# Performance work log

Measured on AMD Instinct MI355X. Metric: run time of the kernel, lower is better.

The kernel has to match this reference:

```python
import jax, jax.numpy as jnp
import numpy as np

B, S, HID, NH, HD, RD, RATIO = 2, 4096, 2048, 16, 128, 64, 4
THETA = 10000.0


def _rope_tables(positions, rd, theta):
    # Unique per-pair frequencies: first half of the Llama cat([freqs, freqs], -1).
    half = rd // 2
    inv_freq = 1.0 / (theta ** (jnp.arange(half, dtype=jnp.float32) / half))
    ang = positions.astype(jnp.float32)[:, None] * inv_freq[None, :]  # [L, half]
    return jnp.cos(ang), jnp.sin(ang)


def _apply_partial_rope_interleaved(x, cos, sin, rd):
    # x: [B, H, L, D]; rotate last rd dims, pairs (2k, 2k+1). cos/sin: [L, rd//2]
    nope, rope = x[..., :-rd], x[..., -rd:]
    pr = rope.reshape(rope.shape[:-1] + (rd // 2, 2))
    a, b = pr[..., 0], pr[..., 1]
    c = cos[None, None]  # [1,1,L,half]
    s = sin[None, None]
    new = jnp.stack([a * c - b * s, a * s + b * c], axis=-1).reshape(rope.shape)
    return jnp.concatenate([nope, new], axis=-1)


def _pool_overlap(kv, gate, ape, ratio, hd):
    # kv/gate: [B, L, 2*hd]; ape: [ratio, 2*hd]. Softmax-gated sum-pool with
    # cross-window overlap: each window pools 2*ratio raw slots (prev window's
    # first-half features + current window's second-half features).
    b, length, feat = kv.shape
    n_w = length // ratio
    kv_w = kv.reshape(b, n_w, ratio, feat)
    gate_w = gate.reshape(b, n_w, ratio, feat) + ape

    def remap(t, fill):
        cur = t[..., hd:]                          # [b, n_w, ratio, hd]
        prev = t[:, :-1, :, :hd]                   # window N-1 first half
        pad = jnp.full((b, 1, ratio, hd), fill, t.dtype)
        prev = jnp.concatenate([pad, prev], axis=1)
        return jnp.concatenate([prev, cur], axis=2)  # [b, n_w, 2*ratio, hd]

    kv_o = remap(kv_w, 0.0)
    gate_o = remap(gate_w, -jnp.inf)
    w = jax.nn.softmax(gate_o, axis=2)
    return (kv_o * w).sum(axis=2)  # [b, n_w, hd]


def setup_inputs() -> dict:
    key = jax.random.key(0)
    ks = jax.random.split(key, 7)
    sc = lambda d: 1.0 / np.sqrt(d)
    return {
        "hidden": jax.random.normal(ks[0], (B, S, HID), jnp.float32),
        "wq": jax.random.normal(ks[1], (HID, NH * HD), jnp.float32) * sc(HID),
        "wkv": jax.random.normal(ks[2], (HID, 2 * HD), jnp.float32) * sc(HID),
        "wgate": jax.random.normal(ks[3], (HID, 2 * HD), jnp.float32) * sc(HID),
        "ape": jax.random.normal(ks[4], (RATIO, 2 * HD), jnp.float32) * 0.02,
        "sinks": jax.random.normal(ks[5], (NH,), jnp.float32) * 0.02,
        "wo": jax.random.normal(ks[6], (NH * HD, HID), jnp.float32) * sc(NH * HD),
        "ratio": RATIO,
        "head_dim": HD,
        "rope_head_dim": RD,
        "num_heads": NH,
    }


def reference(hidden, wq, wkv, wgate, ape, sinks, wo, ratio, head_dim, rope_head_dim, num_heads):
    b, s, _ = hidden.shape
    scale = head_dim ** -0.5

    # Projections
    q = (hidden @ wq).reshape(b, s, num_heads, head_dim).transpose(0, 2, 1, 3)  # [b,h,s,d]
    kv = hidden @ wkv      # [b, s, 2*d]
    gate = hidden @ wgate  # [b, s, 2*d]

    # Overlap gated pooling -> compressed shared KV  [b, n_w, d]
    pooled = _pool_overlap(kv, gate, ape, ratio, head_dim)
    n_w = pooled.shape[1]

    # Partial interleaved RoPE; pooled positions = w * ratio (pool_base = 0)
    q_pos = jnp.arange(s)
    k_pos = jnp.arange(n_w) * ratio
    cq, sq = _rope_tables(q_pos, rope_head_dim, THETA)
    ck, sk = _rope_tables(k_pos, rope_head_dim, THETA)
    q_rot = _apply_partial_rope_interleaved(q, cq, sq, rope_head_dim)
    k_rot = _apply_partial_rope_interleaved(pooled[:, None], ck, sk, rope_head_dim)[:, 0]  # [b,n_w,d]
    v = pooled  # [b, n_w, d]

    # Causal mask over compressed windows: query t sees window w iff its last
    # raw token (w+1)*ratio - 1 <= t.
    mask = jnp.where(q_pos[:, None] >= k_pos[None, :] + ratio - 1, 0.0, -jnp.inf)  # [s, n_w]

    scores = jnp.einsum("bhqd,bkd->bhqk", q_rot, k_rot) * scale + mask[None, None]
    sink_col = jnp.broadcast_to(sinks.reshape(1, num_heads, 1, 1), (b, num_heads, s, 1))
    combined = jnp.concatenate([scores, sink_col], axis=-1)
    probs = jax.nn.softmax(combined - jax.lax.stop_gradient(combined.max(axis=-1, keepdims=True)), axis=-1)[..., :-1]

    attn = jnp.einsum("bhqk,bkd->bhqd", probs, v)               # [b,h,s,d]
    out = attn.transpose(0, 2, 1, 3).reshape(b, s, num_heads * head_dim) @ wo
    return out
```

## Files before the change

### kernel.cpp

```cpp
#include <hip/hip_runtime.h>
#include <math.h>

typedef unsigned short u16;
typedef unsigned int   u32;
typedef __bf16 bf16x8 __attribute__((ext_vector_type(8)));
typedef float  f32x4  __attribute__((ext_vector_type(4)));

#define S_LEN 4096
#define HID   2048
#define NHEAD 16
#define HD    128
#define NW    1024
#define TOK   8192
#define LN10000 9.2103403719761836f
#define NEG_BIG (-1e30f)

__device__ __forceinline__ float b2f(u16 u){
  union { u32 i; float f; } v; v.i = ((u32)u) << 16; return v.f;
}
__device__ __forceinline__ u16 f2b(float f){
  union { float f; u32 i; } v; v.f = f;
  return (u16)((v.i + 0x7FFFu + ((v.i >> 16) & 1u)) >> 16);
}

__global__ __launch_bounds__(256) void cvt_bf16(const float* __restrict__ in,
                                                u16* __restrict__ out){
  size_t i = (size_t)blockIdx.x*256 + threadIdx.x;
  float4 a = ((const float4*)in)[2*i];
  float4 b = ((const float4*)in)[2*i+1];
  u16 t[8];
  t[0]=f2b(a.x); t[1]=f2b(a.y); t[2]=f2b(a.z); t[3]=f2b(a.w);
  t[4]=f2b(b.x); t[5]=f2b(b.y); t[6]=f2b(b.z); t[7]=f2b(b.w);
  *(uint4*)&out[i*8] = *(uint4*)t;
}

__global__ __launch_bounds__(256) void transpose_w(const float* __restrict__ in,
    u16* __restrict__ out, int K, int N){
  __shared__ float t[32][33];
  const int n0 = blockIdx.x*32, k0 = blockIdx.y*32;
  const int c = threadIdx.x & 31, r8 = threadIdx.x >> 5;
  #pragma unroll
  for (int i = 0; i < 4; i++)
    t[r8 + i*8][c] = in[(size_t)(k0 + r8 + i*8)*N + n0 + c];
  __syncthreads();
  #pragma unroll
  for (int i = 0; i < 4; i++)
    out[(size_t)(n0 + r8 + i*8)*K + k0 + c] = f2b(t[c][r8 + i*8]);
}

typedef __attribute__((address_space(3))) u16 as3_u16;
typedef __attribute__((address_space(1))) const u16 as1_u16;
__device__ __forceinline__ void gload16(const u16* g, u16* l){
  __builtin_amdgcn_global_load_lds((as1_u16*)g, (as3_u16*)l, 16, 0, 0);
}

template<typename TC>
__global__ __launch_bounds__(512, 1) void gemm256(const u16* __restrict__ A,
    const u16* __restrict__ Bt, TC* __restrict__ C, int M, int N, int K)
{
  __shared__ __align__(16) u16 LA[2][256*64];
  __shared__ __align__(16) u16 LB[2][256*64];
  const int tid  = threadIdx.x;
  const int lane = tid & 63;
  const int w    = tid >> 6;
  const int wm   = w & 1;
  const int wn   = w >> 1;
  const int lrw  = lane & 15;
  const int quad = lane >> 4;
  const int NB   = N >> 8;
  const int nwg  = gridDim.x;
  const int bid  = blockIdx.x;
  const int swz  = (bid & 7) * (nwg >> 3) + (bid >> 3);
  const int bN   = (swz % NB) << 8;
  const int bM   = (swz / NB) << 8;

  const int rlo = lane >> 3;
  const int csw = ((lane & 7) ^ rlo) << 3;
  const int sr0 = w * 16;
  const int swr = (lrw & 7) << 3;
  const u16* Ag = A  + (size_t)bM * K + (size_t)rlo * K + csw;
  const u16* Bg = Bt + (size_t)bN * K + (size_t)rlo * K + csw;
  const size_t rK = (size_t)K;

  f32x4 acc[8][4];
  #pragma unroll
  for (int i = 0; i < 8; i++)
    #pragma unroll
    for (int j = 0; j < 4; j++)
      #pragma unroll
      for (int r = 0; r < 4; r++) acc[i][j][r] = 0.f;

  const int NT = K >> 6;

  gload16(Ag + (size_t)(  0 + sr0    )*rK, &LA[0][(  0 + sr0    )*64]);
  gload16(Ag + (size_t)(  0 + sr0 + 8)*rK, &LA[0][(  0 + sr0 + 8)*64]);
  gload16(Bg + (size_t)(  0 + sr0    )*rK, &LB[0][(  0 + sr0    )*64]);
  gload16(Bg + (size_t)(  0 + sr0 + 8)*rK, &LB[0][(  0 + sr0 + 8)*64]);
  gload16(Bg + (size_t)(128 + sr0    )*rK, &LB[0][(128 + sr0    )*64]);
  gload16(Bg + (size_t)(128 + sr0 + 8)*rK, &LB[0][(128 + sr0 + 8)*64]);
  gload16(Ag + (size_t)(128 + sr0    )*rK, &LA[0][(128 + sr0    )*64]);
  gload16(Ag + (size_t)(128 + sr0 + 8)*rK, &LA[0][(128 + sr0 + 8)*64]);
  asm volatile("s_waitcnt vmcnt(2)" ::: "memory");
  __builtin_amdgcn_s_barrier();
  __builtin_amdgcn_sched_barrier(0);

  for (int t = 0; t < NT; ++t){
    const int cur = t & 1, nxt = cur ^ 1;
    const int kn  = ((t + 1) & (NT - 1)) << 6;
    const u16* la = &LA[cur][0];
    const u16* lb = &LB[cur][0];
    u16* sa = &LA[nxt][0];
    u16* sb = &LB[nxt][0];

    bf16x8 bfr[4][2], afr[2][2];

    gload16(Ag + (size_t)(  0 + sr0    )*rK + kn, &sa[(  0 + sr0    )*64]);
    gload16(Ag + (size_t)(  0 + sr0 + 8)*rK + kn, &sa[(  0 + sr0 + 8)*64]);
    gload16(Bg + (size_t)(  0 + sr0    )*rK + kn, &sb[(  0 + sr0    )*64]);
    gload16(Bg + (size_t)(  0 + sr0 + 8)*rK + kn, &sb[(  0 + sr0 + 8)*64]);
    #pragma unroll
    for (int nf = 0; nf < 4; nf++)
      #pragma unroll
      for (int kh = 0; kh < 2; kh++)
        bfr[nf][kh] = *(const bf16x8*)&lb[(wn*16 + nf*64 + lrw)*64 + ((kh*32 + quad*8) ^ swr)];
    #pragma unroll
    for (int i = 0; i < 2; i++)
      #pragma unroll
      for (int kh = 0; kh < 2; kh++)
        afr[i][kh] = *(const bf16x8*)&la[(wm*16 + (0+i)*32 + lrw)*64 + ((kh*32 + quad*8) ^ swr)];
    __builtin_amdgcn_s_barrier();
    __builtin_amdgcn_sched_barrier(0);
    __builtin_amdgcn_s_setprio(1);
    #pragma unroll
    for (int i = 0; i < 2; i++)
      #pragma unroll
      for (int nf = 0; nf < 4; nf++)
        #pragma unroll
        for (int kh = 0; kh < 2; kh++)
          acc[0+i][nf] = __builtin_amdgcn_mfma_f32_16x16x32_bf16(afr[i][kh], bfr[nf][kh], acc[0+i][nf], 0, 0, 0);
    __builtin_amdgcn_s_setprio(0);
    __builtin_amdgcn_s_barrier();
    __builtin_amdgcn_sched_barrier(0);

    gload16(Bg + (size_t)(128 + sr0    )*rK + kn, &sb[(128 + sr0    )*64]);
    gload16(Bg + (size_t)(128 + sr0 + 8)*rK + kn, &sb[(128 + sr0 + 8)*64]);
    #pragma unroll
    for (int i = 0; i < 2; i++)
      #pragma unroll
      for (int kh = 0; kh < 2; kh++)
        afr[i][kh] = *(const bf16x8*)&la[(wm*16 + (2+i)*32 + lrw)*64 + ((kh*32 + quad*8) ^ swr)];
    asm volatile("s_waitcnt vmcnt(6)" ::: "memory");
    __builtin_amdgcn_s_barrier();
    __builtin_amdgcn_sched_barrier(0);
    __builtin_amdgcn_s_setprio(1);
    #pragma unroll
    for (int i = 0; i < 2; i++)
      #pragma unroll
      for (int nf = 0; nf < 4; nf++)
        #pragma unroll
        for (int kh = 0; kh < 2; kh++)
          acc[2+i][nf] = __builtin_amdgcn_mfma_f32_16x16x32_bf16(afr[i][kh], bfr[nf][kh], acc[2+i][nf], 0, 0, 0);
    __builtin_amdgcn_s_setprio(0);
    __builtin_amdgcn_s_barrier();
    __builtin_amdgcn_sched_barrier(0);

    gload16(Ag + (size_t)(128 + sr0    )*rK + kn, &sa[(128 + sr0    )*64]);
    gload16(Ag + (size_t)(128 + sr0 + 8)*rK + kn, &sa[(128 + sr0 + 8)*64]);
    #pragma unroll
    for (int i = 0; i < 2; i++)
      #pragma unroll
      for (int kh = 0; kh < 2; kh++)
        afr[i][kh] = *(const bf16x8*)&la[(wm*16 + (4+i)*32 + lrw)*64 + ((kh*32 + quad*8) ^ swr)];
    __builtin_amdgcn_s_barrier();
    __builtin_amdgcn_sched_barrier(0);
    __builtin_amdgcn_s_setprio(1);
    #pragma unroll
    for (int i = 0; i < 2; i++)
      #pragma unroll
      for (int nf = 0; nf < 4; nf++)
        #pragma unroll
        for (int kh = 0; kh < 2; kh++)
          acc[4+i][nf] = __builtin_amdgcn_mfma_f32_16x16x32_bf16(afr[i][kh], bfr[nf][kh], acc[4+i][nf], 0, 0, 0);
    __builtin_amdgcn_s_setprio(0);
    __builtin_amdgcn_s_barrier();
    __builtin_amdgcn_sched_barrier(0);

    #pragma unroll
    for (int i = 0; i < 2; i++)
      #pragma unroll
      for (int kh = 0; kh < 2; kh++)
        afr[i][kh] = *(const bf16x8*)&la[(wm*16 + (6+i)*32 + lrw)*64 + ((kh*32 + quad*8) ^ swr)];
    asm volatile("s_waitcnt vmcnt(2)" ::: "memory");
    __builtin_amdgcn_s_barrier();
    __builtin_amdgcn_sched_barrier(0);
    __builtin_amdgcn_s_setprio(1);
    #pragma unroll
    for (int i = 0; i < 2; i++)
      #pragma unroll
      for (int nf = 0; nf < 4; nf++)
        #pragma unroll
        for (int kh = 0; kh < 2; kh++)
          acc[6+i][nf] = __builtin_amdgcn_mfma_f32_16x16x32_bf16(afr[i][kh], bfr[nf][kh], acc[6+i][nf], 0, 0, 0);
    __builtin_amdgcn_s_setprio(0);
    __builtin_amdgcn_s_barrier();
    __builtin_amdgcn_sched_barrier(0);
  }

  asm volatile("s_waitcnt vmcnt(0)" ::: "memory");

  #pragma unroll
  for (int mf = 0; mf < 8; mf++){
    const int orow0 = bM + wm*16 + mf*32 + quad*4;
    #pragma unroll
    for (int nf = 0; nf < 4; nf++){
      const int ocol = bN + wn*16 + nf*64 + lrw;
      #pragma unroll
      for (int r = 0; r < 4; r++){
        size_t idx = (size_t)(orow0 + r)*N + ocol;
        if constexpr (sizeof(TC) == 4) C[idx] = acc[mf][nf][r];
        else                           C[idx] = f2b(acc[mf][nf][r]);
      }
    }
  }
}

template<typename TC>
__global__ __launch_bounds__(256) void gemm_bf16(const u16* __restrict__ A,
    const u16* __restrict__ Bt, TC* __restrict__ C, int M, int N, int K)
{
  __shared__ u16 As[128*32];
  __shared__ u16 Bs[128*32];
  const int tid  = threadIdx.x;
  const int bM   = blockIdx.y * 128;
  const int bN   = blockIdx.x * 128;
  const int lane = tid & 63;
  const int w    = tid >> 6;
  const int wm   = w >> 1, wn = w & 1;
  const int lrow = lane & 15, quad = lane >> 4;
  const int srow = lane >> 2, skc = (lane & 3) * 8;

  const u16* Ab = &A [(size_t)(bM + w*32 + srow)*K + skc];
  const u16* Bb = &Bt[(size_t)(bN + w*32 + srow)*K + skc];
  const size_t row16 = (size_t)16 * K;

  f32x4 acc[4][4];
  #pragma unroll
  for (int i = 0; i < 4; i++)
    #pragma unroll
    for (int j = 0; j < 4; j++)
      #pragma unroll
      for (int r = 0; r < 4; r++) acc[i][j][r] = 0.f;

  for (int k0 = 0; k0 < K; k0 += 32){
    gload16(Ab + k0,         &As[(w*32     )*32]);
    gload16(Ab + k0 + row16, &As[(w*32 + 16)*32]);
    gload16(Bb + k0,         &Bs[(w*32     )*32]);
    gload16(Bb + k0 + row16, &Bs[(w*32 + 16)*32]);
    __syncthreads();

    bf16x8 af[4], bfv[4];
    #pragma unroll
    for (int mf = 0; mf < 4; mf++)
      af[mf] = *(const bf16x8*)&As[(wm*64 + mf*16 + lrow)*32 + quad*8];
    #pragma unroll
    for (int nf = 0; nf < 4; nf++)
      bfv[nf] = *(const bf16x8*)&Bs[(wn*64 + nf*16 + lrow)*32 + quad*8];
    #pragma unroll
    for (int mf = 0; mf < 4; mf++)
      #pragma unroll
      for (int nf = 0; nf < 4; nf++)
        acc[mf][nf] = __builtin_amdgcn_mfma_f32_16x16x32_bf16(af[mf], bfv[nf], acc[mf][nf], 0, 0, 0);
    __syncthreads();
  }
  #pragma unroll
  for (int mf = 0; mf < 4; mf++){
    #pragma unroll
    for (int nf = 0; nf < 4; nf++){
      int gcol = bN + wn*64 + nf*16 + lrow;
      #pragma unroll
      for (int r = 0; r < 4; r++){
        int grow = bM + wm*64 + mf*16 + quad*4 + r;
        size_t idx = (size_t)grow*N + gcol;
        if constexpr (sizeof(TC) == 4) C[idx] = acc[mf][nf][r];
        else                           C[idx] = f2b(acc[mf][nf][r]);
      }
    }
  }
}

template<typename TA, typename TC>
__global__ __launch_bounds__(256) void gemm_any(const TA* __restrict__ A,
    const float* __restrict__ Bw, TC* __restrict__ C, int M, int N, int K)
{
  __shared__ u16 As[128*40];
  __shared__ u16 Bs[128*40];
  const int tid  = threadIdx.x;
  const int bM   = blockIdx.y * 128;
  const int bN   = blockIdx.x * 128;
  const int lane = tid & 63;
  const int wid  = tid >> 6;
  const int wm   = wid >> 1, wn = wid & 1;
  const int lrow = lane & 15, quad = lane >> 4;

  f32x4 acc[4][4];
  #pragma unroll
  for (int i = 0; i < 4; i++)
    #pragma unroll
    for (int j = 0; j < 4; j++)
      #pragma unroll
      for (int r = 0; r < 4; r++) acc[i][j][r] = 0.f;

  for (int k0 = 0; k0 < K; k0 += 32){
    #pragma unroll
    for (int i = 0; i < 4; i++){
      int c = tid + i*256;
      int row = c >> 3, kc = (c & 7) * 4;
      u16 tmp[4];
      if constexpr (sizeof(TA) == 4){
        float4 v = *(const float4*)&A[(size_t)(bM + row)*K + k0 + kc];
        tmp[0] = f2b(v.x); tmp[1] = f2b(v.y); tmp[2] = f2b(v.z); tmp[3] = f2b(v.w);
      } else {
        *(uint2*)tmp = *(const uint2*)&A[(size_t)(bM + row)*K + k0 + kc];
      }
      *(uint2*)&As[row*40 + kc] = *(uint2*)tmp;
    }
    #pragma unroll
    for (int i = 0; i < 4; i++){
      int c = tid + i*256;
      int kr = c >> 5, nc = (c & 31) * 4;
      float4 v = *(const float4*)&Bw[(size_t)(k0 + kr)*N + bN + nc];
      Bs[(nc+0)*40 + kr] = f2b(v.x);
      Bs[(nc+1)*40 + kr] = f2b(v.y);
      Bs[(nc+2)*40 + kr] = f2b(v.z);
      Bs[(nc+3)*40 + kr] = f2b(v.w);
    }
    __syncthreads();
    bf16x8 af[4], bfv[4];
    #pragma unroll
    for (int mf = 0; mf < 4; mf++)
      af[mf] = *(const bf16x8*)&As[(wm*64 + mf*16 + lrow)*40 + quad*8];
    #pragma unroll
    for (int nf = 0; nf < 4; nf++)
      bfv[nf] = *(const bf16x8*)&Bs[(wn*64 + nf*16 + lrow)*40 + quad*8];
    #pragma unroll
    for (int mf = 0; mf < 4; mf++)
      #pragma unroll
      for (int nf = 0; nf < 4; nf++)
        acc[mf][nf] = __builtin_amdgcn_mfma_f32_16x16x32_bf16(af[mf], bfv[nf], acc[mf][nf], 0, 0, 0);
    __syncthreads();
  }
  #pragma unroll
  for (int mf = 0; mf < 4; mf++){
    #pragma unroll
    for (int nf = 0; nf < 4; nf++){
      int gcol = bN + wn*64 + nf*16 + lrow;
      #pragma unroll
      for (int r = 0; r < 4; r++){
        int grow = bM + wm*64 + mf*16 + quad*4 + r;
        size_t idx = (size_t)grow*N + gcol;
        if constexpr (sizeof(TC) == 4) C[idx] = acc[mf][nf][r];
        else                           C[idx] = f2b(acc[mf][nf][r]);
      }
    }
  }
}

__global__ void rope_q_kernel(u16* __restrict__ q){
  int gid = blockIdx.x * 256 + threadIdx.x;
  int t = gid >> 9;
  int r = gid & 511;
  int h = r >> 5;
  int i = r & 31;
  int pos = t & (S_LEN - 1);
  float freq = expf(-(float)i * (LN10000 / 32.f));
  float ang = (float)pos * freq;
  float sn, cs;
  sincosf(ang, &sn, &cs);
  size_t off = (size_t)t*HID + h*HD + 64 + 2*i;
  float a  = b2f(q[off]);
  float bb = b2f(q[off+1]);
  q[off]   = f2b(a*cs - bb*sn);
  q[off+1] = f2b(a*sn + bb*cs);
}

__global__ void pool_rope_k(const u16* __restrict__ kv, const u16* __restrict__ gate,
                            const float* __restrict__ ape, u16* __restrict__ krot,
                            u16* __restrict__ vT, int str){
  const int d = threadIdx.x;
  const int w = blockIdx.x;
  const int b = blockIdx.y;
  __shared__ float sh[HD];
  const bool hasprev = (w > 0);
  float gc[4], vc[4], gp[4], vp[4];
  float m = NEG_BIG;
  #pragma unroll
  for (int r = 0; r < 4; r++){
    size_t t = (size_t)(b*S_LEN + w*4 + r)*str;
    vc[r] = b2f(kv[t + 128 + d]);
    gc[r] = b2f(gate[t + 128 + d]) + ape[r*256 + 128 + d];
    m = fmaxf(m, gc[r]);
  }
  if (hasprev){
    #pragma unroll
    for (int r = 0; r < 4; r++){
      size_t t = (size_t)(b*S_LEN + (w-1)*4 + r)*str;
      vp[r] = b2f(kv[t + d]);
      gp[r] = b2f(gate[t + d]) + ape[r*256 + d];
      m = fmaxf(m, gp[r]);
    }
  }
  float s = 0.f, acc = 0.f;
  #pragma unroll
  for (int r = 0; r < 4; r++){
    float e = __expf(gc[r] - m); s += e; acc += e*vc[r];
  }
  if (hasprev){
    #pragma unroll
    for (int r = 0; r < 4; r++){
      float e = __expf(gp[r] - m); s += e; acc += e*vp[r];
    }
  }
  float pooled = acc / s;
  sh[d] = pooled;
  __syncthreads();
  float kr = pooled;
  if (d >= 64){
    int i = (d - 64) >> 1;
    float freq = expf(-(float)i * (LN10000 / 32.f));
    float ang = (float)(4*w) * freq;
    float sn, cs;
    sincosf(ang, &sn, &cs);
    if ((d & 1) == 0) kr = sh[d]*cs - sh[d+1]*sn;
    else              kr = sh[d-1]*sn + sh[d]*cs;
  }
  krot[(size_t)(b*NW + w)*HD + d] = f2b(kr);
  vT[(size_t)(b*HD + d)*NW + w]   = f2b(pooled);
}

#define AQT 128
#define AKT 64
#define AKSTR 136
#define AVSTR 72
#define APSTR 72
#define ATT_SCALE 0.088388347648318447f

__global__ __launch_bounds__(256, 2) void attn_kernel(
    const u16* __restrict__ qbuf, const u16* __restrict__ krot,
    const u16* __restrict__ vT, const float* __restrict__ sinks,
    u16* __restrict__ attnbuf)
{
  __shared__ u16 Ks[AKT*AKSTR];
  __shared__ u16 Vt[HD*AVSTR];
  __shared__ u16 Pq[AQT*APSTR];

  const int tid  = threadIdx.x;
  const int q0   = (int)(gridDim.x - 1 - blockIdx.x) * AQT;
  const int h    = blockIdx.y;
  const int b    = blockIdx.z;
  const int lane = tid & 63;
  const int wq   = tid >> 6;
  const int lrw  = lane & 15;
  const int quad = lane >> 4;
  const int qg0  = q0 + wq*32 + lrw;

  bf16x8 qf[2][4];
  #pragma unroll
  for (int g = 0; g < 2; g++){
    const u16* qrow = &qbuf[(size_t)(b*S_LEN + qg0 + g*16)*HID + h*HD];
    #pragma unroll
    for (int d0 = 0; d0 < 4; d0++)
      qf[g][d0] = *(const bf16x8*)&qrow[d0*32 + quad*8];
  }

  float m_run[2] = {NEG_BIG, NEG_BIG};
  float l_run[2] = {0.f, 0.f};
  f32x4 accO[2][8];
  #pragma unroll
  for (int g = 0; g < 2; g++)
    #pragma unroll
    for (int ds = 0; ds < 8; ds++)
      #pragma unroll
      for (int r = 0; r < 4; r++) accO[g][ds][r] = 0.f;

  const int kmax_tile = (q0 + AQT - 1 - 3) >> 2;
  int nchunk = (kmax_tile >> 6) + 1;
  if (nchunk > NW/AKT) nchunk = NW/AKT;

  for (int ch = 0; ch < nchunk; ch++){
    const int kc0 = ch * AKT;
    #pragma unroll
    for (int i = 0; i < 4; i++){
      int c = tid + i*256;
      int kl = c >> 4, cc = (c & 15) * 8;
      *(uint4*)&Ks[kl*AKSTR + cc] =
        *(const uint4*)&krot[(size_t)(b*NW + kc0 + kl)*HD + cc];
    }
    #pragma unroll
    for (int i = 0; i < 4; i++){
      int c = tid + i*256;
      int dv = c >> 3, cc = (c & 7) * 8;
      *(uint4*)&Vt[dv*AVSTR + cc] =
        *(const uint4*)&vT[(size_t)(b*HD + dv)*NW + kc0 + cc];
    }
    __syncthreads();

    f32x4 accS[2][4];
    #pragma unroll
    for (int g = 0; g < 2; g++)
      #pragma unroll
      for (int ks = 0; ks < 4; ks++)
        #pragma unroll
        for (int r = 0; r < 4; r++) accS[g][ks][r] = 0.f;
    #pragma unroll
    for (int d0 = 0; d0 < 4; d0++){
      #pragma unroll
      for (int ks = 0; ks < 4; ks++){
        bf16x8 kf = *(const bf16x8*)&Ks[(ks*16 + lrw)*AKSTR + d0*32 + quad*8];
        accS[0][ks] = __builtin_amdgcn_mfma_f32_16x16x32_bf16(kf, qf[0][d0], accS[0][ks], 0, 0, 0);
        accS[1][ks] = __builtin_amdgcn_mfma_f32_16x16x32_bf16(kf, qf[1][d0], accS[1][ks], 0, 0, 0);
      }
    }

    float alpha[2];
    #pragma unroll
    for (int g = 0; g < 2; g++){
      const int qg = qg0 + g*16;
      float p[16];
      float lmax = NEG_BIG;
      #pragma unroll
      for (int ks = 0; ks < 4; ks++)
        #pragma unroll
        for (int r = 0; r < 4; r++){
          int kg = kc0 + ks*16 + quad*4 + r;
          float s = (qg >= 4*kg + 3) ? accS[g][ks][r]*ATT_SCALE : NEG_BIG;
          p[ks*4 + r] = s;
          lmax = fmaxf(lmax, s);
        }
      lmax = fmaxf(lmax, __shfl_xor(lmax, 16));
      lmax = fmaxf(lmax, __shfl_xor(lmax, 32));
      float mnew = fmaxf(m_run[g], lmax);
      alpha[g] = __expf(m_run[g] - mnew);
      m_run[g] = mnew;
      float ls = 0.f;
      #pragma unroll
      for (int i = 0; i < 16; i++){
        float e = __expf(p[i] - mnew);
        p[i] = e; ls += e;
      }
      ls += __shfl_xor(ls, 16);
      ls += __shfl_xor(ls, 32);
      l_run[g] = l_run[g]*alpha[g] + ls;
      #pragma unroll
      for (int ks = 0; ks < 4; ks++){
        u16 pb[4];
        #pragma unroll
        for (int r = 0; r < 4; r++) pb[r] = f2b(p[ks*4 + r]);
        *(uint2*)&Pq[(wq*32 + g*16 + lrw)*APSTR + ks*16 + quad*4] = *(uint2*)pb;
      }
    }

    #pragma unroll
    for (int g = 0; g < 2; g++)
      #pragma unroll
      for (int ds = 0; ds < 8; ds++)
        #pragma unroll
        for (int r = 0; r < 4; r++) accO[g][ds][r] *= alpha[g];

    #pragma unroll
    for (int kks = 0; kks < 2; kks++){
      bf16x8 pf0 = *(const bf16x8*)&Pq[(wq*32      + lrw)*APSTR + kks*32 + quad*8];
      bf16x8 pf1 = *(const bf16x8*)&Pq[(wq*32 + 16 + lrw)*APSTR + kks*32 + quad*8];
      #pragma unroll
      for (int ds = 0; ds < 8; ds++){
        bf16x8 av = *(const bf16x8*)&Vt[(ds*16 + lrw)*AVSTR + kks*32 + quad*8];
        accO[0][ds] = __builtin_amdgcn_mfma_f32_16x16x32_bf16(av, pf0, accO[0][ds], 0, 0, 0);
        accO[1][ds] = __builtin_amdgcn_mfma_f32_16x16x32_bf16(av, pf1, accO[1][ds], 0, 0, 0);
      }
    }
    __syncthreads();
  }

  const float snk = sinks[h];
  #pragma unroll
  for (int g = 0; g < 2; g++){
    float mf = fmaxf(m_run[g], snk);
    float em = __expf(m_run[g] - mf);
    float sc = em / (l_run[g]*em + __expf(snk - mf));
    size_t o = (size_t)(b*S_LEN + qg0 + g*16)*HID + h*HD;
    #pragma unroll
    for (int ds = 0; ds < 8; ds++){
      u16 ob[4];
      #pragma unroll
      for (int r = 0; r < 4; r++) ob[r] = f2b(accO[g][ds][r] * sc);
      *(uint2*)&attnbuf[o + ds*16 + quad*4] = *(uint2*)ob;
    }
  }
}

extern "C" void kernel_launch(void* const* d_in, const int* in_sizes, int n_in,
                              void* d_out, int out_size, void* d_ws, size_t ws_size,
                              hipStream_t stream)
{
  const float* hidden = (const float*)d_in[0];
  const float* wq     = (const float*)d_in[1];
  const float* wkv    = (const float*)d_in[2];
  const float* wgate  = (const float*)d_in[3];
  const float* ape    = (const float*)d_in[4];
  const float* sinks  = (const float*)d_in[5];
  const float* wo     = (const float*)d_in[6];

  const size_t NEED = ((size_t)TOK*HID*2 + (size_t)TOK*512 + (size_t)4*NW*HD
                     + (size_t)HID*HID + (size_t)512*HID) * sizeof(u16);

  if (ws_size >= NEED){
    u16* hid_bf = (u16*)d_ws;
    u16* qbuf   = hid_bf + (size_t)TOK*HID;
    u16* kvg    = qbuf   + (size_t)TOK*HID;
    u16* krot   = kvg    + (size_t)TOK*512;
    u16* vTb    = krot   + (size_t)2*NW*HD;
    u16* wqT    = vTb    + (size_t)2*NW*HD;
    u16* wkvgT  = wqT    + (size_t)HID*HID;
    u16* attnbuf = hid_bf;
    u16* woT     = kvg;

    cvt_bf16<<<(TOK*HID/8)/256, 256, 0, stream>>>(hidden, hid_bf);
    transpose_w<<<dim3(HID/32, HID/32), 256, 0, stream>>>(wq, wqT, HID, HID);
    transpose_w<<<dim3(256/32, HID/32), 256, 0, stream>>>(wkv,   wkvgT,            HID, 256);
    transpose_w<<<dim3(256/32, HID/32), 256, 0, stream>>>(wgate, wkvgT + (size_t)256*HID, HID, 256);
    gemm256<u16><<<dim3((TOK/256)*(HID/256)), 512, 0, stream>>>(hid_bf, wqT, qbuf, TOK, HID, HID);
    gemm_bf16<u16><<<dim3(512/128, TOK/128), 256, 0, stream>>>(hid_bf, wkvgT, kvg,  TOK, 512, HID);
    rope_q_kernel<<<(TOK*NHEAD*32)/256, 256, 0, stream>>>(qbuf);
    pool_rope_k<<<dim3(NW, 2), 128, 0, stream>>>(kvg, kvg + 256, ape, krot, vTb, 512);
    attn_kernel<<<dim3(S_LEN/AQT, NHEAD, 2), 256, 0, stream>>>(qbuf, krot, vTb, sinks, attnbuf);
    transpose_w<<<dim3(HID/32, HID/32), 256, 0, stream>>>(wo, woT, HID, HID);
    gemm256<float><<<dim3((TOK/256)*(HID/256)), 512, 0, stream>>>(attnbuf, woT, (float*)d_out, TOK, HID, HID);
  } else {
    u16* qbuf    = (u16*)d_ws;
    u16* kvbuf   = qbuf    + (size_t)TOK*HID;
    u16* gatebuf = kvbuf   + (size_t)TOK*256;
    u16* krot    = gatebuf + (size_t)TOK*256;
    u16* vTb     = krot    + (size_t)2*NW*HD;
    u16* attnbuf = vTb     + (size_t)2*NW*HD;

    gemm_any<float,u16><<<dim3(HID/128, TOK/128), 256, 0, stream>>>(hidden, wq,    qbuf,    TOK, HID, HID);
    gemm_any<float,u16><<<dim3(256/128, TOK/128), 256, 0, stream>>>(hidden, wkv,   kvbuf,   TOK, 256, HID);
    gemm_any<float,u16><<<dim3(256/128, TOK/128), 256, 0, stream>>>(hidden, wgate, gatebuf, TOK, 256, HID);
    rope_q_kernel<<<(TOK*NHEAD*32)/256, 256, 0, stream>>>(qbuf);
    pool_rope_k<<<dim3(NW, 2), 128, 0, stream>>>(kvbuf, gatebuf, ape, krot, vTb, 256);
    attn_kernel<<<dim3(S_LEN/AQT, NHEAD, 2), 256, 0, stream>>>(qbuf, krot, vTb, sinks, attnbuf);
    gemm_any<u16,float><<<dim3(HID/128, TOK/128), 256, 0, stream>>>(attnbuf, wo, (float*)d_out, TOK, HID, HID);
  }
}
```

Baseline: 505.1 us.

## Fuse Q RoPE into attention load and register-prefetch next K/V chunk

Removes the standalone rope_q_kernel and applies the interleaved rotary embedding to Q while the attention kernel loads Q fragments into registers. This avoids one full read-modify-write pass over the 32 MB bf16 Q buffer and one launch. The attention main loop also gains a software pipeline: it loads the first K/V chunk before the loop and, inside the loop, fetches the next chunk into registers during compute, then writes them to shared memory after the barrier. The cost is higher register pressure from the prefetch buffers and the sincos work, which could lower occupancy.

```diff
diff --git a/kernel.cpp b/kernel.cpp
--- a/kernel.cpp
+++ b/kernel.cpp
@@ -365,24 +365,6 @@
   }
 }
 
-__global__ void rope_q_kernel(u16* __restrict__ q){
-  int gid = blockIdx.x * 256 + threadIdx.x;
-  int t = gid >> 9;
-  int r = gid & 511;
-  int h = r >> 5;
-  int i = r & 31;
-  int pos = t & (S_LEN - 1);
-  float freq = expf(-(float)i * (LN10000 / 32.f));
-  float ang = (float)pos * freq;
-  float sn, cs;
-  sincosf(ang, &sn, &cs);
-  size_t off = (size_t)t*HID + h*HD + 64 + 2*i;
-  float a  = b2f(q[off]);
-  float bb = b2f(q[off+1]);
-  q[off]   = f2b(a*cs - bb*sn);
-  q[off+1] = f2b(a*sn + bb*cs);
-}
-
 __global__ void pool_rope_k(const u16* __restrict__ kv, const u16* __restrict__ gate,
                             const float* __restrict__ ape, u16* __restrict__ krot,
                             u16* __restrict__ vT, int str){
@@ -467,9 +449,27 @@
   #pragma unroll
   for (int g = 0; g < 2; g++){
     const u16* qrow = &qbuf[(size_t)(b*S_LEN + qg0 + g*16)*HID + h*HD];
-    #pragma unroll
-    for (int d0 = 0; d0 < 4; d0++)
-      qf[g][d0] = *(const bf16x8*)&qrow[d0*32 + quad*8];
+    qf[g][0] = *(const bf16x8*)&qrow[0*32 + quad*8];
+    qf[g][1] = *(const bf16x8*)&qrow[1*32 + quad*8];
+    const float pos = (float)(qg0 + g*16);
+    #pragma unroll
+    for (int d0 = 2; d0 < 4; d0++){
+      u16 raw[8];
+      *(uint4*)raw = *(const uint4*)&qrow[d0*32 + quad*8];
+      u16 outv[8];
+      #pragma unroll
+      for (int pr = 0; pr < 4; pr++){
+        int i = (d0 - 2)*16 + quad*4 + pr;
+        float fr = expf(-(float)i * (LN10000/32.f));
+        float sn, cs;
+        sincosf(pos * fr, &sn, &cs);
+        float a  = b2f(raw[2*pr]);
+        float bb = b2f(raw[2*pr + 1]);
+        outv[2*pr]     = f2b(a*cs - bb*sn);
+        outv[2*pr + 1] = f2b(a*sn + bb*cs);
+      }
+      qf[g][d0] = *(bf16x8*)outv;
+    }
   }
 
   float m_run[2] = {NEG_BIG, NEG_BIG};
@@ -486,23 +486,30 @@
   int nchunk = (kmax_tile >> 6) + 1;
   if (nchunk > NW/AKT) nchunk = NW/AKT;
 
+  #pragma unroll
+  for (int i = 0; i < 4; i++){
+    int c = tid + i*256;
+    uint4 k0v = *(const uint4*)&krot[(size_t)(b*NW + (c >> 4))*HD + (c & 15)*8];
+    uint4 v0v = *(const uint4*)&vT[(size_t)(b*HD + (c >> 3))*NW + (c & 7)*8];
+    *(uint4*)&Ks[(c >> 4)*AKSTR + (c & 15)*8] = k0v;
+    *(uint4*)&Vt[(c >> 3)*AVSTR + (c & 7)*8]  = v0v;
+  }
+
   for (int ch = 0; ch < nchunk; ch++){
     const int kc0 = ch * AKT;
-    #pragma unroll
-    for (int i = 0; i < 4; i++){
-      int c = tid + i*256;
-      int kl = c >> 4, cc = (c & 15) * 8;
-      *(uint4*)&Ks[kl*AKSTR + cc] =
-        *(const uint4*)&krot[(size_t)(b*NW + kc0 + kl)*HD + cc];
-    }
-    #pragma unroll
-    for (int i = 0; i < 4; i++){
-      int c = tid + i*256;
-      int dv = c >> 3, cc = (c & 7) * 8;
-      *(uint4*)&Vt[dv*AVSTR + cc] =
-        *(const uint4*)&vT[(size_t)(b*HD + dv)*NW + kc0 + cc];
-    }
     __syncthreads();
+
+    const bool pf = (ch + 1 < nchunk);
+    uint4 krg[4], vrg[4];
+    if (pf){
+      const int kn = kc0 + AKT;
+      #pragma unroll
+      for (int i = 0; i < 4; i++){
+        int c = tid + i*256;
+        krg[i] = *(const uint4*)&krot[(size_t)(b*NW + kn + (c >> 4))*HD + (c & 15)*8];
+        vrg[i] = *(const uint4*)&vT[(size_t)(b*HD + (c >> 3))*NW + kn + (c & 7)*8];
+      }
+    }
 
     f32x4 accS[2][4];
     #pragma unroll
@@ -578,6 +585,15 @@
       }
     }
     __syncthreads();
+
+    if (pf){
+      #pragma unroll
+      for (int i = 0; i < 4; i++){
+        int c = tid + i*256;
+        *(uint4*)&Ks[(c >> 4)*AKSTR + (c & 15)*8] = krg[i];
+        *(uint4*)&Vt[(c >> 3)*AVSTR + (c & 7)*8]  = vrg[i];
+      }
+    }
   }
 
   const float snk = sinks[h];
@@ -629,7 +645,6 @@
     transpose_w<<<dim3(256/32, HID/32), 256, 0, stream>>>(wgate, wkvgT + (size_t)256*HID, HID, 256);
     gemm256<u16><<<dim3((TOK/256)*(HID/256)), 512, 0, stream>>>(hid_bf, wqT, qbuf, TOK, HID, HID);
     gemm_bf16<u16><<<dim3(512/128, TOK/128), 256, 0, stream>>>(hid_bf, wkvgT, kvg,  TOK, 512, HID);
-    rope_q_kernel<<<(TOK*NHEAD*32)/256, 256, 0, stream>>>(qbuf);
     pool_rope_k<<<dim3(NW, 2), 128, 0, stream>>>(kvg, kvg + 256, ape, krot, vTb, 512);
     attn_kernel<<<dim3(S_LEN/AQT, NHEAD, 2), 256, 0, stream>>>(qbuf, krot, vTb, sinks, attnbuf);
     transpose_w<<<dim3(HID/32, HID/32), 256, 0, stream>>>(wo, woT, HID, HID);
@@ -645,7 +660,6 @@
     gemm_any<float,u16><<<dim3(HID/128, TOK/128), 256, 0, stream>>>(hidden, wq,    qbuf,    TOK, HID, HID);
     gemm_any<float,u16><<<dim3(256/128, TOK/128), 256, 0, stream>>>(hidden, wkv,   kvbuf,   TOK, 256, HID);
     gemm_any<float,u16><<<dim3(256/128, TOK/128), 256, 0, stream>>>(hidden, wgate, gatebuf, TOK, 256, HID);
-    rope_q_kernel<<<(TOK*NHEAD*32)/256, 256, 0, stream>>>(qbuf);
     pool_rope_k<<<dim3(NW, 2), 128, 0, stream>>>(kvbuf, gatebuf, ape, krot, vTb, 256);
     attn_kernel<<<dim3(S_LEN/AQT, NHEAD, 2), 256, 0, stream>>>(qbuf, krot, vTb, sinks, attnbuf);
     gemm_any<u16,float><<<dim3(HID/128, TOK/128), 256, 0, stream>>>(attnbuf, wo, (float*)d_out, TOK, HID, HID);
```

Measured after the change: 562.0 us. 11.3% more time.
